# Kernel tuning notes

Hardware: AMD Instinct MI355X
Metric: run time of the kernel (lower is better)

The kernel has to match this reference:

```python
import jax, jax.numpy as jnp
import numpy as np

N_NODES = 20000
N_EDGES = 320000
IN_CH = 512
HID = 128
HEADS = 4
OUT_CH = 256
NEG_SLOPE = 0.2


def _gat_layer(x, edge_index, W, a_src, a_dst, bias, heads, out_ch, concat):
    """PyG GATConv (add_self_loops=True, eval mode: no dropout).
    x: [N, F_in], edge_index: [2, E] (row 0 = src, row 1 = dst).
    Returns (out, alpha) with alpha: [E+N, heads].
    """
    N = x.shape[0]
    h = (x @ W).reshape(N, heads, out_ch)                      # [N, H, C]
    loops = jnp.arange(N, dtype=edge_index.dtype)
    src = jnp.concatenate([edge_index[0], loops])
    dst = jnp.concatenate([edge_index[1], loops])
    a_s = jnp.einsum('nhc,hc->nh', h, a_src)                   # [N, H]
    a_d = jnp.einsum('nhc,hc->nh', h, a_dst)
    e = a_s[src] + a_d[dst]                                    # [E', H]
    e = jnp.where(e > 0, e, NEG_SLOPE * e)                     # LeakyReLU
    # segment softmax over incoming edges of each dst node
    emax = jax.ops.segment_max(e, dst, num_segments=N)
    ex = jnp.exp(e - emax[dst])
    denom = jax.ops.segment_sum(ex, dst, num_segments=N)
    alpha = ex / denom[dst]                                    # [E', H]
    msg = alpha[:, :, None] * h[src]                           # [E', H, C]
    out = jax.ops.segment_sum(msg, dst, num_segments=N)        # [N, H, C]
    out = out.reshape(N, heads * out_ch) if concat else out.mean(axis=1)
    return out + bias, alpha


def setup_inputs() -> dict:
    key = jax.random.key(0)
    ks = jax.random.split(key, 10)
    s = 0.05
    x = jax.random.normal(ks[0], (N_NODES, IN_CH), dtype=jnp.float32)
    edge_index = jax.random.randint(ks[1], (2, N_EDGES), 0, N_NODES, dtype=jnp.int32)
    W1 = jax.random.normal(ks[2], (IN_CH, HEADS * HID), dtype=jnp.float32) * s
    a_src1 = jax.random.normal(ks[3], (HEADS, HID), dtype=jnp.float32) * s
    a_dst1 = jax.random.normal(ks[4], (HEADS, HID), dtype=jnp.float32) * s
    b1 = jnp.zeros((HEADS * HID,), dtype=jnp.float32)
    W2 = jax.random.normal(ks[5], (HEADS * HID, OUT_CH), dtype=jnp.float32) * s
    a_src2 = jax.random.normal(ks[6], (1, OUT_CH), dtype=jnp.float32) * s
    a_dst2 = jax.random.normal(ks[7], (1, OUT_CH), dtype=jnp.float32) * s
    b2 = jnp.zeros((OUT_CH,), dtype=jnp.float32)
    return {"x": x, "edge_index": edge_index, "W1": W1, "a_src1": a_src1,
            "a_dst1": a_dst1, "b1": b1, "W2": W2, "a_src2": a_src2,
            "a_dst2": a_dst2, "b2": b2}


def reference(x, edge_index, W1, a_src1, a_dst1, b1, W2, a_src2, a_dst2, b2):
    h, alpha1 = _gat_layer(x, edge_index, W1, a_src1, a_dst1, b1, HEADS, HID, True)
    h = jax.nn.elu(h)
    # dropout inactive in eval mode
    out, alpha2 = _gat_layer(h, edge_index, W2, a_src2, a_dst2, b2, 1, OUT_CH, False)
    return out, alpha1, alpha2
```

## Files before the change

kernel.cpp:

```cpp
#include <hip/hip_runtime.h>
#include <hip/hip_bf16.h>
#include <cstdint>


#define NNODES 20000
#define NEDGES 320000
#define ETOT   340000
#define F1     512
#define F2     256
#define HEADS  4

typedef __bf16 bf16;
typedef __attribute__((ext_vector_type(8))) __bf16 bf16x8;
typedef __attribute__((ext_vector_type(4))) float f32x4;

__device__ __forceinline__ float bflo(unsigned p) { return __uint_as_float(p << 16); }
__device__ __forceinline__ float bfhi(unsigned p) { return __uint_as_float(p & 0xffff0000u); }

__device__ __forceinline__ void gload_lds16(const void* g, void* l) {
    __builtin_amdgcn_global_load_lds(
        (const __attribute__((address_space(1))) void*)g,
        (__attribute__((address_space(3))) void*)l, 16, 0, 0);
}

__global__ void deg_count(const int* __restrict__ ei, int* __restrict__ deg) {
    int e = blockIdx.x * blockDim.x + threadIdx.x;
    if (e >= ETOT) return;
    int dst = (e < NEDGES) ? ei[NEDGES + e] : (e - NEDGES);
    atomicAdd(&deg[dst], 1);
}

__global__ void scan_deg(const int* __restrict__ deg, int* __restrict__ offs,
                         int* __restrict__ cur) {
    __shared__ int sums[1024];
    const int t = threadIdx.x;
    const int PER = 20;
    int base = t * PER;
    int local[PER];
    int run = 0;
#pragma unroll
    for (int j = 0; j < PER; j++) {
        int i = base + j;
        int v = (i < NNODES) ? deg[i] : 0;
        local[j] = run;
        run += v;
    }
    sums[t] = run;
    __syncthreads();
    for (int o = 1; o < 1024; o <<= 1) {
        int v = (t >= o) ? sums[t - o] : 0;
        __syncthreads();
        sums[t] += v;
        __syncthreads();
    }
    int texcl = (t == 0) ? 0 : sums[t - 1];
#pragma unroll
    for (int j = 0; j < PER; j++) {
        int i = base + j;
        if (i < NNODES) {
            int e = texcl + local[j];
            cur[i] = e;
            offs[i] = e;
        }
    }
    if (t == 1023) offs[NNODES] = sums[1023];
}

__global__ void fill_csr(const int* __restrict__ ei, int* __restrict__ cur,
                         int* __restrict__ csr_src, int* __restrict__ csr_eid) {
    int e = blockIdx.x * blockDim.x + threadIdx.x;
    if (e >= ETOT) return;
    int src, dst;
    if (e < NEDGES) { src = ei[e]; dst = ei[NEDGES + e]; }
    else            { src = dst = e - NEDGES; }
    int p = atomicAdd(&cur[dst], 1);
    csr_src[p] = src;
    csr_eid[p] = e;
}

__global__ void swizzle_w(const float* __restrict__ W, bf16* __restrict__ Wh,
                          bf16* __restrict__ Wl, int K, int N) {
    int idx = blockIdx.x * blockDim.x + threadIdx.x;
    int total = (K * N) >> 3;
    if (idx >= total) return;
    int lane = idx & 63;
    int tile = idx >> 6;
    int NT = N >> 4;
    int kt = tile / NT, nt = tile - kt * NT;
    int krow = kt * 32 + (lane >> 4) * 8;
    int col  = nt * 16 + (lane & 15);
    union { bf16 b[8]; uint4 u; } hi, lo;
#pragma unroll
    for (int j = 0; j < 8; j++) {
        float w = W[(size_t)(krow + j) * N + col];
        bf16 h = (bf16)w;
        hi.b[j] = h;
        lo.b[j] = (bf16)(w - (float)h);
    }
    *(uint4*)(Wh + (size_t)idx * 8) = hi.u;
    *(uint4*)(Wl + (size_t)idx * 8) = lo.u;
}

__global__ void split_f32(const float* __restrict__ X, bf16* __restrict__ Xh,
                          bf16* __restrict__ Xl, int total8) {
    int i = blockIdx.x * blockDim.x + threadIdx.x;
    if (i >= total8) return;
    float v[8];
    *(float4*)(v)     = *(const float4*)(X + (size_t)i * 8);
    *(float4*)(v + 4) = *(const float4*)(X + (size_t)i * 8 + 4);
    union { bf16 b[8]; uint4 u; } h, l;
#pragma unroll
    for (int j = 0; j < 8; j++) {
        bf16 hh = (bf16)v[j];
        h.b[j] = hh;
        l.b[j] = (bf16)(v[j] - (float)hh);
    }
    *(uint4*)(Xh + (size_t)i * 8) = h.u;
    *(uint4*)(Xl + (size_t)i * 8) = l.u;
}

template <int K, int N, int NYB>
__global__ __launch_bounds__(128) void gemm_fused(const bf16* __restrict__ Ah,
                                                  const bf16* __restrict__ Al,
                                                  const bf16* __restrict__ Bh,
                                                  const bf16* __restrict__ Bl,
                                                  bf16* __restrict__ Cb,
                                                  const float* __restrict__ asrc,
                                                  const float* __restrict__ adst,
                                                  float* __restrict__ as_out,
                                                  float* __restrict__ ad_out, int M) {
    __shared__ __align__(16) char smem[2][8192];
    const int lane = threadIdx.x & 63;
    const int wave = threadIdx.x >> 6;
    constexpr int NT = N / 16;
    constexpr int NKT = K / 32;
    constexpr int CH = 8 * NYB;

    const int nb = gridDim.x;
    const int full = (nb / CH) * CH;
    int bx, by;
    {
        int id = blockIdx.x;
        if (id < full) {
            int chunk = id / CH, pos = id % CH;
            bx = chunk * 8 + (pos & 7);
            by = pos >> 3;
        } else {
            int r = id - full;
            int x0 = full / NYB;
            int remx = nb / NYB - x0;
            bx = x0 + r % remx;
            by = r / remx;
        }
    }
    const int row_base = bx * 64 + wave * 32;
    const int colt0 = by * 4;

    const char* hbase = (const char*)Bh + (size_t)colt0 * 1024;
    const char* lbase = (const char*)Bl + (size_t)colt0 * 1024;
    auto stage = [&](int kt, int buf) {
        size_t kb = (size_t)kt * NT * 1024;
#pragma unroll
        for (int q = 0; q < 4; q++) {
            int off = wave * 4096 + q * 1024;
            const char* src = (off < 4096) ? (hbase + kb + off)
                                           : (lbase + kb + (off - 4096));
            gload_lds16(src + lane * 16, &smem[0][0] + buf * 8192 + off);
        }
    };

    int arow0 = row_base + (lane & 15);
    int arow1 = arow0 + 16;
    if (arow0 >= M) arow0 = M - 1;
    if (arow1 >= M) arow1 = M - 1;
    const int ko = (lane >> 4) * 8;
    const bf16* pah0 = Ah + (size_t)arow0 * K + ko;
    const bf16* pal0 = Al + (size_t)arow0 * K + ko;
    const bf16* pah1 = Ah + (size_t)arow1 * K + ko;
    const bf16* pal1 = Al + (size_t)arow1 * K + ko;

    f32x4 acc0[4] = {}, acc1[4] = {};
    bf16x8 ah0 = *(const bf16x8*)pah0;
    bf16x8 al0 = *(const bf16x8*)pal0;
    bf16x8 ah1 = *(const bf16x8*)pah1;
    bf16x8 al1 = *(const bf16x8*)pal1;

    auto body = [&](const char* bb) {
#pragma unroll
        for (int c = 0; c < 4; c++) {
            bf16x8 bh = *(const bf16x8*)(bb + c * 1024 + lane * 16);
            bf16x8 bl = *(const bf16x8*)(bb + 4096 + c * 1024 + lane * 16);
            acc0[c] = __builtin_amdgcn_mfma_f32_16x16x32_bf16(ah0, bh, acc0[c], 0, 0, 0);
            acc1[c] = __builtin_amdgcn_mfma_f32_16x16x32_bf16(ah1, bh, acc1[c], 0, 0, 0);
            acc0[c] = __builtin_amdgcn_mfma_f32_16x16x32_bf16(ah0, bl, acc0[c], 0, 0, 0);
            acc1[c] = __builtin_amdgcn_mfma_f32_16x16x32_bf16(ah1, bl, acc1[c], 0, 0, 0);
            acc0[c] = __builtin_amdgcn_mfma_f32_16x16x32_bf16(al0, bh, acc0[c], 0, 0, 0);
            acc1[c] = __builtin_amdgcn_mfma_f32_16x16x32_bf16(al1, bh, acc1[c], 0, 0, 0);
        }
    };

    stage(0, 0);
    __syncthreads();
    for (int kt = 0; kt < NKT - 1; ++kt) {
        stage(kt + 1, (kt + 1) & 1);
        bf16x8 nah0 = *(const bf16x8*)(pah0 + (kt + 1) * 32);
        bf16x8 nal0 = *(const bf16x8*)(pal0 + (kt + 1) * 32);
        bf16x8 nah1 = *(const bf16x8*)(pah1 + (kt + 1) * 32);
        bf16x8 nal1 = *(const bf16x8*)(pal1 + (kt + 1) * 32);
        body(&smem[0][0] + (kt & 1) * 8192);
        __syncthreads();
        ah0 = nah0; al0 = nal0; ah1 = nah1; al1 = nal1;
    }
    body(&smem[0][0] + ((NKT - 1) & 1) * 8192);

    const int crow0 = row_base + (lane >> 4) * 4;
    const int col15 = lane & 15;
#pragma unroll
    for (int c = 0; c < 4; c++)
#pragma unroll
        for (int r = 0; r < 4; r++) {
            int r0 = crow0 + r, r1 = r0 + 16;
            int cc = (colt0 + c) * 16 + col15;
            if (r0 < M) Cb[(size_t)r0 * N + cc] = (bf16)acc0[c][r];
            if (r1 < M) Cb[(size_t)r1 * N + cc] = (bf16)acc1[c][r];
        }

    float ss0[4] = {}, sd0[4] = {}, ss1[4] = {}, sd1[4] = {};
#pragma unroll
    for (int c = 0; c < 4; c++) {
        int cw = by * 64 + c * 16 + col15;
        float was = asrc[cw];
        float wad = adst[cw];
#pragma unroll
        for (int r = 0; r < 4; r++) {
            ss0[r] += acc0[c][r] * was; sd0[r] += acc0[c][r] * wad;
            ss1[r] += acc1[c][r] * was; sd1[r] += acc1[c][r] * wad;
        }
    }
#pragma unroll
    for (int o = 1; o < 16; o <<= 1)
#pragma unroll
        for (int r = 0; r < 4; r++) {
            ss0[r] += __shfl_xor(ss0[r], o); sd0[r] += __shfl_xor(sd0[r], o);
            ss1[r] += __shfl_xor(ss1[r], o); sd1[r] += __shfl_xor(sd1[r], o);
        }
    if (col15 == 0) {
        constexpr int HS = (N == 512) ? 4 : 1;
        const int head = (N == 512) ? (by >> 1) : 0;
#pragma unroll
        for (int r = 0; r < 4; r++) {
            int r0 = crow0 + r, r1 = r0 + 16;
            if (r0 < M) {
                atomicAdd(&as_out[r0 * HS + head], ss0[r]);
                atomicAdd(&ad_out[r0 * HS + head], sd0[r]);
            }
            if (r1 < M) {
                atomicAdd(&as_out[r1 * HS + head], ss1[r]);
                atomicAdd(&ad_out[r1 * HS + head], sd1[r]);
            }
        }
    }
}

__global__ __launch_bounds__(256) void sm1(const float* __restrict__ as1,
                                           const float* __restrict__ ad1,
                                           const int* __restrict__ offs,
                                           const int* __restrict__ csr_src,
                                           const int* __restrict__ csr_eid,
                                           float* __restrict__ alpha1,
                                           float* __restrict__ ac1) {
    const int lane = threadIdx.x & 63;
    const int n = __builtin_amdgcn_readfirstlane(blockIdx.x * 4 + (threadIdx.x >> 6));
    if (n >= NNODES) return;
    const int beg = offs[n];
    const int deg = offs[n + 1] - beg;

    float4 ad4 = *(const float4*)(ad1 + n * 4);
    const float adn[4] = {ad4.x, ad4.y, ad4.z, ad4.w};

    float ls[4] = {0.f, 0.f, 0.f, 0.f};
    for (int idx = lane; idx < deg; idx += 64) {
        int s = csr_src[beg + idx];
        float4 a4 = *(const float4*)(as1 + s * 4);
        float v[4] = {a4.x + adn[0], a4.y + adn[1], a4.z + adn[2], a4.w + adn[3]};
#pragma unroll
        for (int h = 0; h < 4; h++) {
            v[h] = v[h] > 0.f ? v[h] : 0.2f * v[h];
            ls[h] += __expf(v[h]);
        }
    }
#pragma unroll
    for (int o = 1; o < 64; o <<= 1)
#pragma unroll
        for (int h = 0; h < 4; h++) ls[h] += __shfl_xor(ls[h], o);
    float rden[4];
#pragma unroll
    for (int h = 0; h < 4; h++) rden[h] = 1.f / ls[h];

    for (int idx = lane; idx < deg; idx += 64) {
        int s = csr_src[beg + idx];
        int e = csr_eid[beg + idx];
        float4 a4 = *(const float4*)(as1 + s * 4);
        float v0 = a4.x + adn[0]; v0 = v0 > 0.f ? v0 : 0.2f * v0;
        float v1 = a4.y + adn[1]; v1 = v1 > 0.f ? v1 : 0.2f * v1;
        float v2 = a4.z + adn[2]; v2 = v2 > 0.f ? v2 : 0.2f * v2;
        float v3 = a4.w + adn[3]; v3 = v3 > 0.f ? v3 : 0.2f * v3;
        float al0 = __expf(v0) * rden[0];
        float al1 = __expf(v1) * rden[1];
        float al2 = __expf(v2) * rden[2];
        float al3 = __expf(v3) * rden[3];
        *(float4*)(alpha1 + (size_t)e * 4) = make_float4(al0, al1, al2, al3);
        ac1[0 * ETOT + beg + idx] = al0;
        ac1[1 * ETOT + beg + idx] = al1;
        ac1[2 * ETOT + beg + idx] = al2;
        ac1[3 * ETOT + beg + idx] = al3;
    }
}

__global__ __launch_bounds__(256) void sm2(const float* __restrict__ as2,
                                           const float* __restrict__ ad2,
                                           const int* __restrict__ offs,
                                           const int* __restrict__ csr_src,
                                           const int* __restrict__ csr_eid,
                                           float* __restrict__ alpha2,
                                           float* __restrict__ ac2) {
    const int lane = threadIdx.x & 63;
    const int n = __builtin_amdgcn_readfirstlane(blockIdx.x * 4 + (threadIdx.x >> 6));
    if (n >= NNODES) return;
    const int beg = offs[n];
    const int deg = offs[n + 1] - beg;
    const float adn = ad2[n];

    float ls = 0.f;
    for (int idx = lane; idx < deg; idx += 64) {
        int s = csr_src[beg + idx];
        float v = as2[s] + adn;
        v = v > 0.f ? v : 0.2f * v;
        ls += __expf(v);
    }
#pragma unroll
    for (int o = 1; o < 64; o <<= 1) ls += __shfl_xor(ls, o);
    float rden = 1.f / ls;

    for (int idx = lane; idx < deg; idx += 64) {
        int s = csr_src[beg + idx];
        int e = csr_eid[beg + idx];
        float v = as2[s] + adn;
        v = v > 0.f ? v : 0.2f * v;
        float a = __expf(v) * rden;
        alpha2[e] = a;
        ac2[beg + idx] = a;
    }
}

__global__ __launch_bounds__(256) void agg1(const bf16* __restrict__ h1b,
                                            const float* __restrict__ ac1,
                                            const int* __restrict__ offs,
                                            const int* __restrict__ csr_src,
                                            const float* __restrict__ b1,
                                            bf16* __restrict__ h1eh,
                                            bf16* __restrict__ h1el) {
    const int lane = threadIdx.x & 63;
    const int n = __builtin_amdgcn_readfirstlane(blockIdx.x * 4 + (threadIdx.x >> 6));
    if (n >= NNODES) return;
    const int beg = offs[n];
    const int deg = offs[n + 1] - beg;

    const int myh = lane >> 4;
    const float* ap = ac1 + (size_t)myh * ETOT + beg;
    const bf16* hb = h1b + lane * 8;

    float acc[8] = {};
    int i = 0;
    for (; i + 4 <= deg; i += 4) {
        int s0 = csr_src[beg + i];
        int s1 = csr_src[beg + i + 1];
        int s2 = csr_src[beg + i + 2];
        int s3 = csr_src[beg + i + 3];
        float a0 = ap[i], a1 = ap[i + 1], a2 = ap[i + 2], a3 = ap[i + 3];
        uint4 p0 = *(const uint4*)(hb + (size_t)s0 * F1);
        uint4 p1 = *(const uint4*)(hb + (size_t)s1 * F1);
        uint4 p2 = *(const uint4*)(hb + (size_t)s2 * F1);
        uint4 p3 = *(const uint4*)(hb + (size_t)s3 * F1);
        acc[0] += a0 * bflo(p0.x); acc[1] += a0 * bfhi(p0.x);
        acc[2] += a0 * bflo(p0.y); acc[3] += a0 * bfhi(p0.y);
        acc[4] += a0 * bflo(p0.z); acc[5] += a0 * bfhi(p0.z);
        acc[6] += a0 * bflo(p0.w); acc[7] += a0 * bfhi(p0.w);
        acc[0] += a1 * bflo(p1.x); acc[1] += a1 * bfhi(p1.x);
        acc[2] += a1 * bflo(p1.y); acc[3] += a1 * bfhi(p1.y);
        acc[4] += a1 * bflo(p1.z); acc[5] += a1 * bfhi(p1.z);
        acc[6] += a1 * bflo(p1.w); acc[7] += a1 * bfhi(p1.w);
        acc[0] += a2 * bflo(p2.x); acc[1] += a2 * bfhi(p2.x);
        acc[2] += a2 * bflo(p2.y); acc[3] += a2 * bfhi(p2.y);
        acc[4] += a2 * bflo(p2.z); acc[5] += a2 * bfhi(p2.z);
        acc[6] += a2 * bflo(p2.w); acc[7] += a2 * bfhi(p2.w);
        acc[0] += a3 * bflo(p3.x); acc[1] += a3 * bfhi(p3.x);
        acc[2] += a3 * bflo(p3.y); acc[3] += a3 * bfhi(p3.y);
        acc[4] += a3 * bflo(p3.z); acc[5] += a3 * bfhi(p3.z);
        acc[6] += a3 * bflo(p3.w); acc[7] += a3 * bfhi(p3.w);
    }
    for (; i < deg; i++) {
        int s = csr_src[beg + i];
        float a = ap[i];
        uint4 p = *(const uint4*)(hb + (size_t)s * F1);
        acc[0] += a * bflo(p.x); acc[1] += a * bfhi(p.x);
        acc[2] += a * bflo(p.y); acc[3] += a * bfhi(p.y);
        acc[4] += a * bflo(p.z); acc[5] += a * bfhi(p.z);
        acc[6] += a * bflo(p.w); acc[7] += a * bfhi(p.w);
    }

    const int c8 = lane * 8;
    float bv[8];
    *(float4*)(bv)     = *(const float4*)(b1 + c8);
    *(float4*)(bv + 4) = *(const float4*)(b1 + c8 + 4);
    union { bf16 b[8]; uint4 u; } hh, ll;
#pragma unroll
    for (int j = 0; j < 8; j++) {
        float t = acc[j] + bv[j];
        float o = t > 0.f ? t : expm1f(t);
        bf16 hb2 = (bf16)o;
        hh.b[j] = hb2;
        ll.b[j] = (bf16)(o - (float)hb2);
    }
    *(uint4*)(h1eh + (size_t)n * F1 + c8) = hh.u;
    *(uint4*)(h1el + (size_t)n * F1 + c8) = ll.u;
}

__global__ __launch_bounds__(256) void agg2(const bf16* __restrict__ h2b,
                                            const float* __restrict__ ac2,
                                            const int* __restrict__ offs,
                                            const int* __restrict__ csr_src,
                                            const float* __restrict__ b2,
                                            float* __restrict__ out) {
    const int lane = threadIdx.x & 63;
    const int n = __builtin_amdgcn_readfirstlane(blockIdx.x * 4 + (threadIdx.x >> 6));
    if (n >= NNODES) return;
    const int beg = offs[n];
    const int deg = offs[n + 1] - beg;

    const bf16* hb = h2b + lane * 4;

    float acc[4] = {};
    int i = 0;
    for (; i + 4 <= deg; i += 4) {
        int s0 = csr_src[beg + i];
        int s1 = csr_src[beg + i + 1];
        int s2 = csr_src[beg + i + 2];
        int s3 = csr_src[beg + i + 3];
        float a0 = ac2[beg + i],     a1 = ac2[beg + i + 1];
        float a2 = ac2[beg + i + 2], a3 = ac2[beg + i + 3];
        uint2 p0 = *(const uint2*)(hb + (size_t)s0 * F2);
        uint2 p1 = *(const uint2*)(hb + (size_t)s1 * F2);
        uint2 p2 = *(const uint2*)(hb + (size_t)s2 * F2);
        uint2 p3 = *(const uint2*)(hb + (size_t)s3 * F2);
        acc[0] += a0 * bflo(p0.x); acc[1] += a0 * bfhi(p0.x);
        acc[2] += a0 * bflo(p0.y); acc[3] += a0 * bfhi(p0.y);
        acc[0] += a1 * bflo(p1.x); acc[1] += a1 * bfhi(p1.x);
        acc[2] += a1 * bflo(p1.y); acc[3] += a1 * bfhi(p1.y);
        acc[0] += a2 * bflo(p2.x); acc[1] += a2 * bfhi(p2.x);
        acc[2] += a2 * bflo(p2.y); acc[3] += a2 * bfhi(p2.y);
        acc[0] += a3 * bflo(p3.x); acc[1] += a3 * bfhi(p3.x);
        acc[2] += a3 * bflo(p3.y); acc[3] += a3 * bfhi(p3.y);
    }
    for (; i < deg; i++) {
        int s = csr_src[beg + i];
        float a = ac2[beg + i];
        uint2 p = *(const uint2*)(hb + (size_t)s * F2);
        acc[0] += a * bflo(p.x); acc[1] += a * bfhi(p.x);
        acc[2] += a * bflo(p.y); acc[3] += a * bfhi(p.y);
    }

    const int c4 = lane * 4;
    float4 bv = *(const float4*)(b2 + c4);
    *(float4*)(out + (size_t)n * F2 + c4) =
        make_float4(acc[0] + bv.x, acc[1] + bv.y, acc[2] + bv.z, acc[3] + bv.w);
}

extern "C" void kernel_launch(void* const* d_in, const int* in_sizes, int n_in,
                              void* d_out, int out_size, void* d_ws, size_t ws_size,
                              hipStream_t stream) {
    const float* x      = (const float*)d_in[0];
    const int*   ei     = (const int*)d_in[1];
    const float* W1     = (const float*)d_in[2];
    const float* a_src1 = (const float*)d_in[3];
    const float* a_dst1 = (const float*)d_in[4];
    const float* b1     = (const float*)d_in[5];
    const float* W2     = (const float*)d_in[6];
    const float* a_src2 = (const float*)d_in[7];
    const float* a_dst2 = (const float*)d_in[8];
    const float* b2     = (const float*)d_in[9];

    char* ws = (char*)d_ws;
    size_t off = 0;
    auto alloc = [&](size_t bytes) -> char* {
        char* p = ws + off;
        off += (bytes + 255) & ~(size_t)255;
        return p;
    };
    bf16*  h1b  = (bf16*) alloc((size_t)NNODES * F1 * 2);
    bf16*  h2b  = (bf16*) alloc((size_t)NNODES * F2 * 2);
    bf16*  h1eh = (bf16*) alloc((size_t)NNODES * F1 * 2);
    bf16*  h1el = (bf16*) alloc((size_t)NNODES * F1 * 2);
    bf16*  Xh   = (bf16*) alloc((size_t)NNODES * F1 * 2);
    bf16*  Xl   = (bf16*) alloc((size_t)NNODES * F1 * 2);
    float* as1  = (float*)alloc((size_t)NNODES * 4 * 4);
    float* ad1  = (float*)alloc((size_t)NNODES * 4 * 4);
    float* as2  = (float*)alloc((size_t)NNODES * 4);
    float* ad2  = (float*)alloc((size_t)NNODES * 4);
    float* ac1  = (float*)alloc((size_t)4 * ETOT * 4);
    float* ac2  = (float*)alloc((size_t)ETOT * 4);
    bf16*  W1h  = (bf16*) alloc((size_t)512 * 512 * 2);
    bf16*  W1l  = (bf16*) alloc((size_t)512 * 512 * 2);
    bf16*  W2h  = (bf16*) alloc((size_t)512 * 256 * 2);
    bf16*  W2l  = (bf16*) alloc((size_t)512 * 256 * 2);
    int*   deg  = (int*)  alloc((size_t)NNODES * 4);
    int*   offs = (int*)  alloc((size_t)(NNODES + 1) * 4);
    int*   cur  = (int*)  alloc((size_t)NNODES * 4);
    int*   csrS = (int*)  alloc((size_t)ETOT * 4);
    int*   csrE = (int*)  alloc((size_t)ETOT * 4);

    float* out2   = (float*)d_out;
    float* alpha1 = out2 + (size_t)NNODES * F2;
    float* alpha2 = alpha1 + (size_t)ETOT * HEADS;

    hipMemsetAsync(deg, 0, (size_t)NNODES * 4, stream);
    hipMemsetAsync(as1, 0, (size_t)NNODES * 4 * 4, stream);
    hipMemsetAsync(ad1, 0, (size_t)NNODES * 4 * 4, stream);
    hipMemsetAsync(as2, 0, (size_t)NNODES * 4, stream);
    hipMemsetAsync(ad2, 0, (size_t)NNODES * 4, stream);
    deg_count<<<(ETOT + 255) / 256, 256, 0, stream>>>(ei, deg);
    scan_deg<<<1, 1024, 0, stream>>>(deg, offs, cur);
    fill_csr<<<(ETOT + 255) / 256, 256, 0, stream>>>(ei, cur, csrS, csrE);

    swizzle_w<<<(512 * 512 / 8 + 255) / 256, 256, 0, stream>>>(W1, W1h, W1l, 512, 512);
    swizzle_w<<<(512 * 256 / 8 + 255) / 256, 256, 0, stream>>>(W2, W2h, W2l, 512, 256);
    split_f32<<<(NNODES * F1 / 8 + 255) / 256, 256, 0, stream>>>(
        x, Xh, Xl, NNODES * F1 / 8);

    const int NB = (NNODES + 3) / 4;
    gemm_fused<512, 512, 8><<<313 * 8, 128, 0, stream>>>(
        Xh, Xl, W1h, W1l, h1b, a_src1, a_dst1, as1, ad1, NNODES);
    sm1<<<NB, 256, 0, stream>>>(as1, ad1, offs, csrS, csrE, alpha1, ac1);
    agg1<<<NB, 256, 0, stream>>>(h1b, ac1, offs, csrS, b1, h1eh, h1el);

    gemm_fused<512, 256, 4><<<313 * 4, 128, 0, stream>>>(
        h1eh, h1el, W2h, W2l, h2b, a_src2, a_dst2, as2, ad2, NNODES);
    sm2<<<NB, 256, 0, stream>>>(as2, ad2, offs, csrS, csrE, alpha2, ac2);
    agg2<<<NB, 256, 0, stream>>>(h2b, ac2, offs, csrS, b2, out2);
}
```

Baseline: 366.4 us.

## Replace LDS-staged GEMM with single-wave register-tiled 64x64 tile loaded directly

The fused split-bf16 GEMM drops LDS staging and barriers. Each block is now one 64-lane wave that computes a 64x64 output tile with 4x4 MFMA accumulators, loading A and B fragments from global memory straight into registers with a two-deep software prefetch. The five zeroing memsets are merged into one by placing the zeroed buffers contiguously at the start of the workspace. In exchange, register pressure rises sharply (16 accumulators plus double-buffered fragments), so occupancy may drop, and B tiles are no longer shared between waves through LDS.

```diff
diff --git a/kernel.cpp b/kernel.cpp
--- a/kernel.cpp
+++ b/kernel.cpp
@@ -16,12 +16,6 @@
 
 __device__ __forceinline__ float bflo(unsigned p) { return __uint_as_float(p << 16); }
 __device__ __forceinline__ float bfhi(unsigned p) { return __uint_as_float(p & 0xffff0000u); }
-
-__device__ __forceinline__ void gload_lds16(const void* g, void* l) {
-    __builtin_amdgcn_global_load_lds(
-        (const __attribute__((address_space(1))) void*)g,
-        (__attribute__((address_space(3))) void*)l, 16, 0, 0);
-}
 
 __global__ void deg_count(const int* __restrict__ ei, int* __restrict__ deg) {
     int e = blockIdx.x * blockDim.x + threadIdx.x;
@@ -120,18 +114,16 @@
 }
 
 template <int K, int N, int NYB>
-__global__ __launch_bounds__(128) void gemm_fused(const bf16* __restrict__ Ah,
-                                                  const bf16* __restrict__ Al,
-                                                  const bf16* __restrict__ Bh,
-                                                  const bf16* __restrict__ Bl,
-                                                  bf16* __restrict__ Cb,
-                                                  const float* __restrict__ asrc,
-                                                  const float* __restrict__ adst,
-                                                  float* __restrict__ as_out,
-                                                  float* __restrict__ ad_out, int M) {
-    __shared__ __align__(16) char smem[2][8192];
-    const int lane = threadIdx.x & 63;
-    const int wave = threadIdx.x >> 6;
+__global__ __launch_bounds__(64) void gemm_fused(const bf16* __restrict__ Ah,
+                                                 const bf16* __restrict__ Al,
+                                                 const bf16* __restrict__ Bh,
+                                                 const bf16* __restrict__ Bl,
+                                                 bf16* __restrict__ Cb,
+                                                 const float* __restrict__ asrc,
+                                                 const float* __restrict__ adst,
+                                                 float* __restrict__ as_out,
+                                                 float* __restrict__ ad_out, int M) {
+    const int lane = threadIdx.x;
     constexpr int NT = N / 16;
     constexpr int NKT = K / 32;
     constexpr int CH = 8 * NYB;
@@ -153,112 +145,107 @@
             by = r / remx;
         }
     }
-    const int row_base = bx * 64 + wave * 32;
+    const int row_base = bx * 64;
     const int colt0 = by * 4;
 
-    const char* hbase = (const char*)Bh + (size_t)colt0 * 1024;
-    const char* lbase = (const char*)Bl + (size_t)colt0 * 1024;
-    auto stage = [&](int kt, int buf) {
+    const int ko = (lane >> 4) * 8;
+    const bf16* pa[4];
+    const bf16* pl[4];
+#pragma unroll
+    for (int f = 0; f < 4; f++) {
+        int r = row_base + f * 16 + (lane & 15);
+        if (r >= M) r = M - 1;
+        pa[f] = Ah + (size_t)r * K + ko;
+        pl[f] = Al + (size_t)r * K + ko;
+    }
+    const char* bh_base = (const char*)Bh + (size_t)colt0 * 1024 + lane * 16;
+    const char* bl_base = (const char*)Bl + (size_t)colt0 * 1024 + lane * 16;
+
+    f32x4 acc[4][4] = {};
+    bf16x8 bhA[4], blA[4], ahA[4], alA[4];
+    bf16x8 bhB[4], blB[4], ahB[4], alB[4];
+
+    auto loadF = [&](int kt, bf16x8* bh, bf16x8* bl, bf16x8* ah, bf16x8* al) {
         size_t kb = (size_t)kt * NT * 1024;
 #pragma unroll
-        for (int q = 0; q < 4; q++) {
-            int off = wave * 4096 + q * 1024;
-            const char* src = (off < 4096) ? (hbase + kb + off)
-                                           : (lbase + kb + (off - 4096));
-            gload_lds16(src + lane * 16, &smem[0][0] + buf * 8192 + off);
+        for (int c = 0; c < 4; c++) {
+            bh[c] = *(const bf16x8*)(bh_base + kb + c * 1024);
+            bl[c] = *(const bf16x8*)(bl_base + kb + c * 1024);
+        }
+#pragma unroll
+        for (int f = 0; f < 4; f++) {
+            ah[f] = *(const bf16x8*)(pa[f] + kt * 32);
+            al[f] = *(const bf16x8*)(pl[f] + kt * 32);
         }
     };
-
-    int arow0 = row_base + (lane & 15);
-    int arow1 = arow0 + 16;
-    if (arow0 >= M) arow0 = M - 1;
-    if (arow1 >= M) arow1 = M - 1;
-    const int ko = (lane >> 4) * 8;
-    const bf16* pah0 = Ah + (size_t)arow0 * K + ko;
-    const bf16* pal0 = Al + (size_t)arow0 * K + ko;
-    const bf16* pah1 = Ah + (size_t)arow1 * K + ko;
-    const bf16* pal1 = Al + (size_t)arow1 * K + ko;
-
-    f32x4 acc0[4] = {}, acc1[4] = {};
-    bf16x8 ah0 = *(const bf16x8*)pah0;
-    bf16x8 al0 = *(const bf16x8*)pal0;
-    bf16x8 ah1 = *(const bf16x8*)pah1;
-    bf16x8 al1 = *(const bf16x8*)pal1;
-
-    auto body = [&](const char* bb) {
-#pragma unroll
-        for (int c = 0; c < 4; c++) {
-            bf16x8 bh = *(const bf16x8*)(bb + c * 1024 + lane * 16);
-            bf16x8 bl = *(const bf16x8*)(bb + 4096 + c * 1024 + lane * 16);
-            acc0[c] = __builtin_amdgcn_mfma_f32_16x16x32_bf16(ah0, bh, acc0[c], 0, 0, 0);
-            acc1[c] = __builtin_amdgcn_mfma_f32_16x16x32_bf16(ah1, bh, acc1[c], 0, 0, 0);
-            acc0[c] = __builtin_amdgcn_mfma_f32_16x16x32_bf16(ah0, bl, acc0[c], 0, 0, 0);
-            acc1[c] = __builtin_amdgcn_mfma_f32_16x16x32_bf16(ah1, bl, acc1[c], 0, 0, 0);
-            acc0[c] = __builtin_amdgcn_mfma_f32_16x16x32_bf16(al0, bh, acc0[c], 0, 0, 0);
-            acc1[c] = __builtin_amdgcn_mfma_f32_16x16x32_bf16(al1, bh, acc1[c], 0, 0, 0);
-        }
+    auto compute = [&](bf16x8* bh, bf16x8* bl, bf16x8* ah, bf16x8* al) {
+#pragma unroll
+        for (int c = 0; c < 4; c++)
+#pragma unroll
+            for (int f = 0; f < 4; f++) {
+                acc[f][c] = __builtin_amdgcn_mfma_f32_16x16x32_bf16(ah[f], bh[c], acc[f][c], 0, 0, 0);
+                acc[f][c] = __builtin_amdgcn_mfma_f32_16x16x32_bf16(ah[f], bl[c], acc[f][c], 0, 0, 0);
+                acc[f][c] = __builtin_amdgcn_mfma_f32_16x16x32_bf16(al[f], bh[c], acc[f][c], 0, 0, 0);
+            }
     };
 
-    stage(0, 0);
-    __syncthreads();
-    for (int kt = 0; kt < NKT - 1; ++kt) {
-        stage(kt + 1, (kt + 1) & 1);
-        bf16x8 nah0 = *(const bf16x8*)(pah0 + (kt + 1) * 32);
-        bf16x8 nal0 = *(const bf16x8*)(pal0 + (kt + 1) * 32);
-        bf16x8 nah1 = *(const bf16x8*)(pah1 + (kt + 1) * 32);
-        bf16x8 nal1 = *(const bf16x8*)(pal1 + (kt + 1) * 32);
-        body(&smem[0][0] + (kt & 1) * 8192);
-        __syncthreads();
-        ah0 = nah0; al0 = nal0; ah1 = nah1; al1 = nal1;
-    }
-    body(&smem[0][0] + ((NKT - 1) & 1) * 8192);
-
-    const int crow0 = row_base + (lane >> 4) * 4;
+    loadF(0, bhA, blA, ahA, alA);
+    for (int kt = 0; kt < NKT; kt += 2) {
+        loadF(kt + 1, bhB, blB, ahB, alB);
+        compute(bhA, blA, ahA, alA);
+        if (kt + 2 < NKT) loadF(kt + 2, bhA, blA, ahA, alA);
+        compute(bhB, blB, ahB, alB);
+    }
+
     const int col15 = lane & 15;
-#pragma unroll
-    for (int c = 0; c < 4; c++)
-#pragma unroll
-        for (int r = 0; r < 4; r++) {
-            int r0 = crow0 + r, r1 = r0 + 16;
-            int cc = (colt0 + c) * 16 + col15;
-            if (r0 < M) Cb[(size_t)r0 * N + cc] = (bf16)acc0[c][r];
-            if (r1 < M) Cb[(size_t)r1 * N + cc] = (bf16)acc1[c][r];
-        }
-
-    float ss0[4] = {}, sd0[4] = {}, ss1[4] = {}, sd1[4] = {};
+    const int rsub = (lane >> 4) * 4;
+#pragma unroll
+    for (int f = 0; f < 4; f++)
+#pragma unroll
+        for (int c = 0; c < 4; c++)
+#pragma unroll
+            for (int r = 0; r < 4; r++) {
+                int rr = row_base + f * 16 + rsub + r;
+                int cc = (colt0 + c) * 16 + col15;
+                if (rr < M) Cb[(size_t)rr * N + cc] = (bf16)acc[f][c][r];
+            }
+
+    float ss[4][4] = {}, sd[4][4] = {};
 #pragma unroll
     for (int c = 0; c < 4; c++) {
         int cw = by * 64 + c * 16 + col15;
         float was = asrc[cw];
         float wad = adst[cw];
 #pragma unroll
-        for (int r = 0; r < 4; r++) {
-            ss0[r] += acc0[c][r] * was; sd0[r] += acc0[c][r] * wad;
-            ss1[r] += acc1[c][r] * was; sd1[r] += acc1[c][r] * wad;
-        }
+        for (int f = 0; f < 4; f++)
+#pragma unroll
+            for (int r = 0; r < 4; r++) {
+                ss[f][r] += acc[f][c][r] * was;
+                sd[f][r] += acc[f][c][r] * wad;
+            }
     }
 #pragma unroll
     for (int o = 1; o < 16; o <<= 1)
 #pragma unroll
-        for (int r = 0; r < 4; r++) {
-            ss0[r] += __shfl_xor(ss0[r], o); sd0[r] += __shfl_xor(sd0[r], o);
-            ss1[r] += __shfl_xor(ss1[r], o); sd1[r] += __shfl_xor(sd1[r], o);
-        }
+        for (int f = 0; f < 4; f++)
+#pragma unroll
+            for (int r = 0; r < 4; r++) {
+                ss[f][r] += __shfl_xor(ss[f][r], o);
+                sd[f][r] += __shfl_xor(sd[f][r], o);
+            }
     if (col15 == 0) {
         constexpr int HS = (N == 512) ? 4 : 1;
         const int head = (N == 512) ? (by >> 1) : 0;
 #pragma unroll
-        for (int r = 0; r < 4; r++) {
-            int r0 = crow0 + r, r1 = r0 + 16;
-            if (r0 < M) {
-                atomicAdd(&as_out[r0 * HS + head], ss0[r]);
-                atomicAdd(&ad_out[r0 * HS + head], sd0[r]);
+        for (int f = 0; f < 4; f++)
+#pragma unroll
+            for (int r = 0; r < 4; r++) {
+                int rr = row_base + f * 16 + rsub + r;
+                if (rr < M) {
+                    atomicAdd(&as_out[rr * HS + head], ss[f][r]);
+                    atomicAdd(&ad_out[rr * HS + head], sd[f][r]);
+                }
             }
-            if (r1 < M) {
-                atomicAdd(&as_out[r1 * HS + head], ss1[r]);
-                atomicAdd(&ad_out[r1 * HS + head], sd1[r]);
-            }
-        }
     }
 }
 
@@ -497,23 +484,26 @@
         off += (bytes + 255) & ~(size_t)255;
         return p;
     };
+    char*  zbase = ws;
+    int*   deg  = (int*)  alloc((size_t)NNODES * 4);
+    float* as1  = (float*)alloc((size_t)NNODES * 4 * 4);
+    float* ad1  = (float*)alloc((size_t)NNODES * 4 * 4);
+    float* as2  = (float*)alloc((size_t)NNODES * 4);
+    float* ad2  = (float*)alloc((size_t)NNODES * 4);
+    size_t zlen = off;
+
     bf16*  h1b  = (bf16*) alloc((size_t)NNODES * F1 * 2);
     bf16*  h2b  = (bf16*) alloc((size_t)NNODES * F2 * 2);
     bf16*  h1eh = (bf16*) alloc((size_t)NNODES * F1 * 2);
     bf16*  h1el = (bf16*) alloc((size_t)NNODES * F1 * 2);
     bf16*  Xh   = (bf16*) alloc((size_t)NNODES * F1 * 2);
     bf16*  Xl   = (bf16*) alloc((size_t)NNODES * F1 * 2);
-    float* as1  = (float*)alloc((size_t)NNODES * 4 * 4);
-    float* ad1  = (float*)alloc((size_t)NNODES * 4 * 4);
-    float* as2  = (float*)alloc((size_t)NNODES * 4);
-    float* ad2  = (float*)alloc((size_t)NNODES * 4);
     float* ac1  = (float*)alloc((size_t)4 * ETOT * 4);
     float* ac2  = (float*)alloc((size_t)ETOT * 4);
     bf16*  W1h  = (bf16*) alloc((size_t)512 * 512 * 2);
     bf16*  W1l  = (bf16*) alloc((size_t)512 * 512 * 2);
     bf16*  W2h  = (bf16*) alloc((size_t)512 * 256 * 2);
     bf16*  W2l  = (bf16*) alloc((size_t)512 * 256 * 2);
-    int*   deg  = (int*)  alloc((size_t)NNODES * 4);
     int*   offs = (int*)  alloc((size_t)(NNODES + 1) * 4);
     int*   cur  = (int*)  alloc((size_t)NNODES * 4);
     int*   csrS = (int*)  alloc((size_t)ETOT * 4);
@@ -523,11 +513,7 @@
     float* alpha1 = out2 + (size_t)NNODES * F2;
     float* alpha2 = alpha1 + (size_t)ETOT * HEADS;
 
-    hipMemsetAsync(deg, 0, (size_t)NNODES * 4, stream);
-    hipMemsetAsync(as1, 0, (size_t)NNODES * 4 * 4, stream);
-    hipMemsetAsync(ad1, 0, (size_t)NNODES * 4 * 4, stream);
-    hipMemsetAsync(as2, 0, (size_t)NNODES * 4, stream);
-    hipMemsetAsync(ad2, 0, (size_t)NNODES * 4, stream);
+    hipMemsetAsync(zbase, 0, zlen, stream);
     deg_count<<<(ETOT + 255) / 256, 256, 0, stream>>>(ei, deg);
     scan_deg<<<1, 1024, 0, stream>>>(deg, offs, cur);
     fill_csr<<<(ETOT + 255) / 256, 256, 0, stream>>>(ei, cur, csrS, csrE);
@@ -538,12 +524,12 @@
         x, Xh, Xl, NNODES * F1 / 8);
 
     const int NB = (NNODES + 3) / 4;
-    gemm_fused<512, 512, 8><<<313 * 8, 128, 0, stream>>>(
+    gemm_fused<512, 512, 8><<<313 * 8, 64, 0, stream>>>(
         Xh, Xl, W1h, W1l, h1b, a_src1, a_dst1, as1, ad1, NNODES);
     sm1<<<NB, 256, 0, stream>>>(as1, ad1, offs, csrS, csrE, alpha1, ac1);
     agg1<<<NB, 256, 0, stream>>>(h1b, ac1, offs, csrS, b1, h1eh, h1el);
 
-    gemm_fused<512, 256, 4><<<313 * 4, 128, 0, stream>>>(
+    gemm_fused<512, 256, 4><<<313 * 4, 64, 0, stream>>>(
         h1eh, h1el, W2h, W2l, h2b, a_src2, a_dst2, as2, ad2, NNODES);
     sm2<<<NB, 256, 0, stream>>>(as2, ad2, offs, csrS, csrE, alpha2, ac2);
     agg2<<<NB, 256, 0, stream>>>(h2b, ac2, offs, csrS, b2, out2);
```

Result: no change. 368.0 us (+0.4%).
